# Optimization experiments

Measured on AMD Instinct MI355X. Metric: run time of the kernel, lower is better.

## Reference

```python
import jax, jax.numpy as jnp
import numpy as np

N_NODES = 50000
N_EDGES = 600000
D_IN = 128
D = 128
N_REL = 2
N_LAYERS = 3


def rgcn_conv(h, src, dst, edge_type, weight, root, bias):
    # PyG RGCNConv (no bases), aggr='mean' per relation:
    # out_i = h_i @ root + bias + sum_r mean_{j in N_r(i)} h_j @ W_r
    out = h @ root + bias                      # [N, D]
    hs = h[src]                                # [E, D] gather once
    for r in range(N_REL):
        mask = (edge_type == r).astype(h.dtype)          # [E]
        agg = jax.ops.segment_sum(hs * mask[:, None], dst, num_segments=N_NODES)  # [N, D]
        cnt = jax.ops.segment_sum(mask, dst, num_segments=N_NODES)                # [N]
        mean = agg / jnp.maximum(cnt, 1.0)[:, None]
        out = out + mean @ weight[r]
    return out


def setup_inputs() -> dict:
    key = jax.random.key(0)
    ks = jax.random.split(key, 10)
    x = jax.random.normal(ks[0], (N_NODES, D_IN), dtype=jnp.float32)
    edge_index = jax.random.randint(ks[1], (2, N_EDGES), 0, N_NODES, dtype=jnp.int64)
    edge_attr = jax.random.normal(ks[2], (N_EDGES, N_REL), dtype=jnp.float32)
    # input projection f: Linear(D_IN, D); stored as [D_IN, D] (apply as x @ Wf + bf)
    Wf = jax.random.normal(ks[3], (D_IN, D), dtype=jnp.float32) / np.sqrt(D_IN)
    bf = jnp.zeros((D,), dtype=jnp.float32)
    # per-layer RGCNConv params, stacked over layers
    conv_weight = jax.random.normal(ks[4], (N_LAYERS, N_REL, D, D), dtype=jnp.float32) / np.sqrt(D)
    conv_root = jax.random.normal(ks[5], (N_LAYERS, D, D), dtype=jnp.float32) / np.sqrt(D)
    conv_bias = jnp.zeros((N_LAYERS, D), dtype=jnp.float32)
    return {"x": x, "edge_index": edge_index, "edge_attr": edge_attr,
            "Wf": Wf, "bf": bf, "conv_weight": conv_weight,
            "conv_root": conv_root, "conv_bias": conv_bias}


def reference(x, edge_index, edge_attr, Wf, bf, conv_weight, conv_root, conv_bias):
    src, dst = edge_index[0], edge_index[1]
    edge_type = jnp.argmax(edge_attr, axis=1)           # [E]
    h = jax.nn.relu(x @ Wf + bf)                        # [N, D]
    for l in range(N_LAYERS):
        h = rgcn_conv(h, src, dst, edge_type, conv_weight[l], conv_root[l], conv_bias[l])
        h = jax.nn.relu(h)
    return h
```

## Files before the change

### kernel.cpp

```cpp
#include <hip/hip_runtime.h>
#include <hip/hip_bf16.h>

#define NN 50000
#define NE 600000
#define D 128
#define NREL 2
#define BM 128

typedef __attribute__((ext_vector_type(8))) short bf16x8;
typedef __attribute__((ext_vector_type(4))) float f32x4;

__device__ __forceinline__ float bf2f(short s) {
    return __uint_as_float(((unsigned int)(unsigned short)s) << 16);
}

__global__ void k_etype_count(const float* __restrict__ attr,
                              const int* __restrict__ dst,
                              int* __restrict__ etype,
                              int* __restrict__ cnt, int E) {
    int i = blockIdx.x * blockDim.x + threadIdx.x;
    if (i >= E) return;
    float2 a = reinterpret_cast<const float2*>(attr)[i];
    int r = (a.y > a.x) ? 1 : 0;
    etype[i] = r;
    atomicAdd(&cnt[r * NN + dst[i]], 1);
}

__global__ void k_inv(const int* __restrict__ cnt, float* __restrict__ inv) {
    int i = blockIdx.x * blockDim.x + threadIdx.x;
    if (i >= NREL * NN) return;
    int c = cnt[i];
    inv[i] = 1.0f / (float)(c > 1 ? c : 1);
}

__global__ void k_alloc(const int* __restrict__ cnt, int* __restrict__ off,
                        int* __restrict__ total) {
    int i = blockIdx.x * blockDim.x + threadIdx.x;
    if (i >= NREL * NN) return;
    off[i] = atomicAdd(total, cnt[i]);
}

__global__ void k_fill(const int* __restrict__ src, const int* __restrict__ dst,
                       const int* __restrict__ etype,
                       int* __restrict__ cursor, int* __restrict__ srcs, int E) {
    int i = blockIdx.x * blockDim.x + threadIdx.x;
    if (i >= E) return;
    int key = etype[i] * NN + dst[i];
    int pos = atomicAdd(&cursor[key], 1);
    srcs[pos] = src[i];
}

__global__ void k_cvt_x(const float* __restrict__ x,
                        __hip_bfloat16* __restrict__ xb, int n4) {
    int i = blockIdx.x * blockDim.x + threadIdx.x;
    if (i >= n4) return;
    float4 v = reinterpret_cast<const float4*>(x)[i];
    __hip_bfloat162 a = __float22bfloat162_rn(make_float2(v.x, v.y));
    __hip_bfloat162 b = __float22bfloat162_rn(make_float2(v.z, v.w));
    reinterpret_cast<__hip_bfloat162*>(xb)[i * 2 + 0] = a;
    reinterpret_cast<__hip_bfloat162*>(xb)[i * 2 + 1] = b;
}

__global__ void k_prep_w(const float* __restrict__ Wf,
                         const float* __restrict__ cw,
                         const float* __restrict__ cr,
                         __hip_bfloat16* __restrict__ wt) {
    int idx = blockIdx.x * blockDim.x + threadIdx.x;
    if (idx >= 16384 + 3 * 49152) return;
    float v;
    if (idx < 16384) {
        int n = idx >> 7, k = idx & 127;
        v = Wf[k * 128 + n];
    } else {
        int j = idx - 16384;
        int l = j / 49152; j %= 49152;
        int n = j / 384, k = j % 384;
        if (k < 128)      v = cr[((size_t)l * 128 + k) * 128 + n];
        else if (k < 256) v = cw[((size_t)(l * 2 + 0) * 128 + (k - 128)) * 128 + n];
        else              v = cw[((size_t)(l * 2 + 1) * 128 + (k - 256)) * 128 + n];
    }
    wt[idx] = __float2bfloat16(v);
}

__global__ __launch_bounds__(256)
void k_aggregate(const __hip_bfloat16* __restrict__ h,
                 const int* __restrict__ srcs,
                 const int* __restrict__ off, const int* __restrict__ cnt,
                 const float* __restrict__ inv,
                 __hip_bfloat16* __restrict__ agg) {
    int wid = (blockIdx.x * blockDim.x + threadIdx.x) >> 6;
    int lane = threadIdx.x & 63;
    if (wid >= NREL * NN) return;
    int start = off[wid], c = cnt[wid];
    int g = lane >> 4, l16 = lane & 15;

    int sv = (lane < c) ? srcs[start + lane] : 0;

    float acc[8];
#pragma unroll
    for (int i = 0; i < 8; i++) acc[i] = 0.f;

    for (int base = 0; base < c; base += 8) {
        int j0 = base + g, j1 = base + g + 4;
        int t0 = __shfl(sv, j0 & 63);
        int t1 = __shfl(sv, j1 & 63);
        int s0 = (j0 < 64) ? t0 : ((j0 < c) ? srcs[start + j0] : 0);
        int s1 = (j1 < 64) ? t1 : ((j1 < c) ? srcs[start + j1] : 0);
        if (j0 < c) {
            bf16x8 v0 = *reinterpret_cast<const bf16x8*>(
                h + (size_t)s0 * D + l16 * 8);
#pragma unroll
            for (int i = 0; i < 8; i++) acc[i] += bf2f(v0[i]);
        }
        if (j1 < c) {
            bf16x8 v1 = *reinterpret_cast<const bf16x8*>(
                h + (size_t)s1 * D + l16 * 8);
#pragma unroll
            for (int i = 0; i < 8; i++) acc[i] += bf2f(v1[i]);
        }
    }

#pragma unroll
    for (int i = 0; i < 8; i++) acc[i] += __shfl_xor(acc[i], 16);
#pragma unroll
    for (int i = 0; i < 8; i++) acc[i] += __shfl_xor(acc[i], 32);

    if (g == 0) {
        float sc = inv[wid];
        union { bf16x8 v; __hip_bfloat162 h2[4]; } o;
#pragma unroll
        for (int i = 0; i < 4; i++)
            o.h2[i] = __float22bfloat162_rn(
                make_float2(acc[2 * i] * sc, acc[2 * i + 1] * sc));
        *reinterpret_cast<bf16x8*>(agg + (size_t)wid * D + l16 * 8) = o.v;
    }
}

template <int KTOT, bool OUT_F32>
__global__ __launch_bounds__(256)
void k_gemm_mfma(const __hip_bfloat16* __restrict__ A0,
                 const __hip_bfloat16* __restrict__ A1,
                 const __hip_bfloat16* __restrict__ A2,
                 const __hip_bfloat16* __restrict__ Wt,
                 const float* __restrict__ bias,
                 void* __restrict__ outv, int N) {
    __shared__ uint4 sB4[1024];
    char* sB = (char*)sB4;
    const int tid = threadIdx.x;
    const int w = tid >> 6;
    const int l16 = tid & 15, lg = (tid & 63) >> 4;
    const __hip_bfloat16* As[3] = {A0, A1, A2};

    f32x4 acc[2][8];
#pragma unroll
    for (int m = 0; m < 2; m++)
#pragma unroll
        for (int n = 0; n < 8; n++) acc[m][n] = (f32x4)(0.f);

    const size_t row0 = (size_t)blockIdx.x * BM;
    const int NKB = KTOT / 64;
#pragma unroll
    for (int kb = 0; kb < NKB; ++kb) {
        const __hip_bfloat16* Ac = As[kb >> 1];
        const int koff = (kb & 1) * 64;
        bf16x8 afr[2][2];
#pragma unroll
        for (int mb = 0; mb < 2; ++mb)
#pragma unroll
            for (int kk = 0; kk < 2; ++kk) {
                int r = (int)row0 + w * 32 + mb * 16 + l16;
                if (r >= N) r = N - 1;
                afr[mb][kk] = *reinterpret_cast<const bf16x8*>(
                    Ac + (size_t)r * D + koff + kk * 32 + lg * 8);
            }
        __syncthreads();
        {
            int trow = tid >> 3;
            int tb = (tid & 7) * 16;
#pragma unroll
            for (int p = 0; p < 4; ++p) {
                int rr = trow + p * 32;
                uint4 v = *reinterpret_cast<const uint4*>(
                    (const char*)(Wt + (size_t)rr * KTOT + kb * 64) + tb);
                *reinterpret_cast<uint4*>(sB + rr * 128 + (tb ^ ((rr & 7) << 4))) = v;
            }
        }
        __syncthreads();
#pragma unroll
        for (int kk = 0; kk < 2; ++kk) {
#pragma unroll
            for (int nb = 0; nb < 8; ++nb) {
                int brow = nb * 16 + l16;
                int bcol = kk * 64 + lg * 16;
                bf16x8 bfr = *reinterpret_cast<const bf16x8*>(
                    sB + brow * 128 + (bcol ^ ((brow & 7) << 4)));
                acc[0][nb] = __builtin_amdgcn_mfma_f32_16x16x32_bf16(
                    afr[0][kk], bfr, acc[0][nb], 0, 0, 0);
                acc[1][nb] = __builtin_amdgcn_mfma_f32_16x16x32_bf16(
                    afr[1][kk], bfr, acc[1][nb], 0, 0, 0);
            }
        }
    }
#pragma unroll
    for (int nb = 0; nb < 8; ++nb) {
        int n = nb * 16 + l16;
        float bv = bias[n];
#pragma unroll
        for (int mb = 0; mb < 2; ++mb) {
#pragma unroll
            for (int r = 0; r < 4; ++r) {
                long grow = (long)row0 + w * 32 + mb * 16 + lg * 4 + r;
                if (grow < N) {
                    float v = acc[mb][nb][r] + bv;
                    v = v > 0.f ? v : 0.f;
                    if (OUT_F32)
                        ((float*)outv)[(size_t)grow * D + n] = v;
                    else
                        ((__hip_bfloat16*)outv)[(size_t)grow * D + n] =
                            __float2bfloat16(v);
                }
            }
        }
    }
}

extern "C" void kernel_launch(void* const* d_in, const int* in_sizes, int n_in,
                              void* d_out, int out_size, void* d_ws, size_t ws_size,
                              hipStream_t stream) {
    const float* x    = (const float*)d_in[0];
    const int*   ei   = (const int*)d_in[1];
    const float* attr = (const float*)d_in[2];
    const float* Wf   = (const float*)d_in[3];
    const float* bf   = (const float*)d_in[4];
    const float* cw   = (const float*)d_in[5];
    const float* cr   = (const float*)d_in[6];
    const float* cb   = (const float*)d_in[7];
    const int* src  = ei;
    const int* dstv = ei + NE;

    char* p = (char*)d_ws;
    __hip_bfloat16* h0   = (__hip_bfloat16*)p; p += (size_t)NN * D * 2;
    __hip_bfloat16* h1   = (__hip_bfloat16*)p; p += (size_t)NN * D * 2;
    __hip_bfloat16* aggb = (__hip_bfloat16*)p; p += (size_t)2 * NN * D * 2;
    __hip_bfloat16* xb   = (__hip_bfloat16*)p; p += (size_t)NN * D * 2;
    __hip_bfloat16* wt   = (__hip_bfloat16*)p; p += (size_t)(16384 + 3 * 49152) * 2;
    float* inv  = (float*)p;                p += (size_t)2 * NN * 4;
    int*   cnt  = (int*)p;                  p += (size_t)2 * NN * 4;
    int*   etyp = (int*)p;                  p += (size_t)NE * 4;
    int*   off  = (int*)p;                  p += (size_t)2 * NN * 4;
    int*   cur  = (int*)p;                  p += (size_t)2 * NN * 4;
    int*   srcs = (int*)p;                  p += (size_t)NE * 4;
    int*   total= (int*)p;

    float* outp = (float*)d_out;

    hipMemsetAsync(cnt, 0, (size_t)2 * NN * sizeof(int), stream);
    hipMemsetAsync(total, 0, sizeof(int), stream);
    k_etype_count<<<(NE + 255) / 256, 256, 0, stream>>>(attr, dstv, etyp, cnt, NE);
    k_inv<<<(2 * NN + 255) / 256, 256, 0, stream>>>(cnt, inv);
    k_alloc<<<(2 * NN + 255) / 256, 256, 0, stream>>>(cnt, off, total);
    hipMemcpyAsync(cur, off, (size_t)2 * NN * sizeof(int),
                   hipMemcpyDeviceToDevice, stream);
    k_fill<<<(NE + 255) / 256, 256, 0, stream>>>(src, dstv, etyp, cur, srcs, NE);
    k_cvt_x<<<(NN * D / 4 + 255) / 256, 256, 0, stream>>>(x, xb, NN * D / 4);
    k_prep_w<<<(16384 + 3 * 49152 + 255) / 256, 256, 0, stream>>>(Wf, cw, cr, wt);

    const int gblocks = (NN + BM - 1) / BM;
    k_gemm_mfma<128, false><<<gblocks, 256, 0, stream>>>(
        xb, xb, xb, wt, bf, h0, NN);

    const int ablocks = (2 * NN * 64 + 255) / 256;
    for (int l = 0; l < 3; ++l) {
        const __hip_bfloat16* hin = (l == 1) ? h1 : h0;
        k_aggregate<<<ablocks, 256, 0, stream>>>(hin, srcs, off, cnt, inv, aggb);
        const __hip_bfloat16* wl = wt + 16384 + (size_t)l * 49152;
        const float* bl = cb + (size_t)l * D;
        if (l == 2) {
            k_gemm_mfma<384, true><<<gblocks, 256, 0, stream>>>(
                hin, aggb, aggb + (size_t)NN * D, wl, bl, outp, NN);
        } else {
            __hip_bfloat16* hout = (l == 0) ? h1 : h0;
            k_gemm_mfma<384, false><<<gblocks, 256, 0, stream>>>(
                hin, aggb, aggb + (size_t)NN * D, wl, bl, hout, NN);
        }
    }
}
```

Baseline: 284.0 us.

## Fuse preprocessing kernels, fold x conversion into projection GEMM, unroll aggregation gathers

Merges edge-type counting with weight prep into one launch, and merges the inverse-count, offset-allocation and cursor copy into a second launch. The edge-type buffer is dropped by recomputing the argmax inside the fill kernel. A dedicated projection GEMM reads fp32 x directly and converts it to bf16 in registers, which removes the separate conversion pass and its bf16 copy of x. The aggregation loop now issues four independent row loads per iteration instead of two to raise memory-level parallelism, at the cost of reading row 0 for masked-out slots.

```diff
diff --git a/kernel.cpp b/kernel.cpp
--- a/kernel.cpp
+++ b/kernel.cpp
@@ -13,73 +13,71 @@
 __device__ __forceinline__ float bf2f(short s) {
     return __uint_as_float(((unsigned int)(unsigned short)s) << 16);
 }
-
-__global__ void k_etype_count(const float* __restrict__ attr,
-                              const int* __restrict__ dst,
-                              int* __restrict__ etype,
-                              int* __restrict__ cnt, int E) {
+__device__ __forceinline__ bf16x8 pack_bf8(const float* a) {
+    union { bf16x8 v; __hip_bfloat162 h2[4]; } o;
+#pragma unroll
+    for (int i = 0; i < 4; i++)
+        o.h2[i] = __float22bfloat162_rn(make_float2(a[2 * i], a[2 * i + 1]));
+    return o.v;
+}
+
+#define NEB ((NE + 255) / 256)
+#define NWT (16384 + 3 * 49152)
+#define NWB ((NWT + 255) / 256)
+
+__global__ void k_pre1(const float* __restrict__ attr,
+                       const int* __restrict__ dst,
+                       int* __restrict__ cnt,
+                       const float* __restrict__ Wf,
+                       const float* __restrict__ cw,
+                       const float* __restrict__ cr,
+                       __hip_bfloat16* __restrict__ wt) {
+    if (blockIdx.x < NEB) {
+        int i = blockIdx.x * blockDim.x + threadIdx.x;
+        if (i >= NE) return;
+        float2 a = reinterpret_cast<const float2*>(attr)[i];
+        int r = (a.y > a.x) ? 1 : 0;
+        atomicAdd(&cnt[r * NN + dst[i]], 1);
+    } else {
+        int idx = (blockIdx.x - NEB) * blockDim.x + threadIdx.x;
+        if (idx >= NWT) return;
+        float v;
+        if (idx < 16384) {
+            int n = idx >> 7, k = idx & 127;
+            v = Wf[k * 128 + n];
+        } else {
+            int j = idx - 16384;
+            int l = j / 49152; j %= 49152;
+            int n = j / 384, k = j % 384;
+            if (k < 128)      v = cr[((size_t)l * 128 + k) * 128 + n];
+            else if (k < 256) v = cw[((size_t)(l * 2 + 0) * 128 + (k - 128)) * 128 + n];
+            else              v = cw[((size_t)(l * 2 + 1) * 128 + (k - 256)) * 128 + n];
+        }
+        wt[idx] = __float2bfloat16(v);
+    }
+}
+
+__global__ void k_pre2(const int* __restrict__ cnt, float* __restrict__ inv,
+                       int* __restrict__ off, int* __restrict__ cur,
+                       int* __restrict__ total) {
+    int i = blockIdx.x * blockDim.x + threadIdx.x;
+    if (i >= NREL * NN) return;
+    int c = cnt[i];
+    inv[i] = 1.0f / (float)(c > 1 ? c : 1);
+    int o = atomicAdd(total, c);
+    off[i] = o;
+    cur[i] = o;
+}
+
+__global__ void k_fill(const float* __restrict__ attr,
+                       const int* __restrict__ src, const int* __restrict__ dst,
+                       int* __restrict__ cursor, int* __restrict__ srcs, int E) {
     int i = blockIdx.x * blockDim.x + threadIdx.x;
     if (i >= E) return;
     float2 a = reinterpret_cast<const float2*>(attr)[i];
     int r = (a.y > a.x) ? 1 : 0;
-    etype[i] = r;
-    atomicAdd(&cnt[r * NN + dst[i]], 1);
-}
-
-__global__ void k_inv(const int* __restrict__ cnt, float* __restrict__ inv) {
-    int i = blockIdx.x * blockDim.x + threadIdx.x;
-    if (i >= NREL * NN) return;
-    int c = cnt[i];
-    inv[i] = 1.0f / (float)(c > 1 ? c : 1);
-}
-
-__global__ void k_alloc(const int* __restrict__ cnt, int* __restrict__ off,
-                        int* __restrict__ total) {
-    int i = blockIdx.x * blockDim.x + threadIdx.x;
-    if (i >= NREL * NN) return;
-    off[i] = atomicAdd(total, cnt[i]);
-}
-
-__global__ void k_fill(const int* __restrict__ src, const int* __restrict__ dst,
-                       const int* __restrict__ etype,
-                       int* __restrict__ cursor, int* __restrict__ srcs, int E) {
-    int i = blockIdx.x * blockDim.x + threadIdx.x;
-    if (i >= E) return;
-    int key = etype[i] * NN + dst[i];
-    int pos = atomicAdd(&cursor[key], 1);
+    int pos = atomicAdd(&cursor[r * NN + dst[i]], 1);
     srcs[pos] = src[i];
-}
-
-__global__ void k_cvt_x(const float* __restrict__ x,
-                        __hip_bfloat16* __restrict__ xb, int n4) {
-    int i = blockIdx.x * blockDim.x + threadIdx.x;
-    if (i >= n4) return;
-    float4 v = reinterpret_cast<const float4*>(x)[i];
-    __hip_bfloat162 a = __float22bfloat162_rn(make_float2(v.x, v.y));
-    __hip_bfloat162 b = __float22bfloat162_rn(make_float2(v.z, v.w));
-    reinterpret_cast<__hip_bfloat162*>(xb)[i * 2 + 0] = a;
-    reinterpret_cast<__hip_bfloat162*>(xb)[i * 2 + 1] = b;
-}
-
-__global__ void k_prep_w(const float* __restrict__ Wf,
-                         const float* __restrict__ cw,
-                         const float* __restrict__ cr,
-                         __hip_bfloat16* __restrict__ wt) {
-    int idx = blockIdx.x * blockDim.x + threadIdx.x;
-    if (idx >= 16384 + 3 * 49152) return;
-    float v;
-    if (idx < 16384) {
-        int n = idx >> 7, k = idx & 127;
-        v = Wf[k * 128 + n];
-    } else {
-        int j = idx - 16384;
-        int l = j / 49152; j %= 49152;
-        int n = j / 384, k = j % 384;
-        if (k < 128)      v = cr[((size_t)l * 128 + k) * 128 + n];
-        else if (k < 256) v = cw[((size_t)(l * 2 + 0) * 128 + (k - 128)) * 128 + n];
-        else              v = cw[((size_t)(l * 2 + 1) * 128 + (k - 256)) * 128 + n];
-    }
-    wt[idx] = __float2bfloat16(v);
 }
 
 __global__ __launch_bounds__(256)
@@ -100,23 +98,24 @@
 #pragma unroll
     for (int i = 0; i < 8; i++) acc[i] = 0.f;
 
-    for (int base = 0; base < c; base += 8) {
-        int j0 = base + g, j1 = base + g + 4;
-        int t0 = __shfl(sv, j0 & 63);
-        int t1 = __shfl(sv, j1 & 63);
-        int s0 = (j0 < 64) ? t0 : ((j0 < c) ? srcs[start + j0] : 0);
-        int s1 = (j1 < 64) ? t1 : ((j1 < c) ? srcs[start + j1] : 0);
-        if (j0 < c) {
-            bf16x8 v0 = *reinterpret_cast<const bf16x8*>(
-                h + (size_t)s0 * D + l16 * 8);
-#pragma unroll
-            for (int i = 0; i < 8; i++) acc[i] += bf2f(v0[i]);
-        }
-        if (j1 < c) {
-            bf16x8 v1 = *reinterpret_cast<const bf16x8*>(
-                h + (size_t)s1 * D + l16 * 8);
-#pragma unroll
-            for (int i = 0; i < 8; i++) acc[i] += bf2f(v1[i]);
+    for (int base = 0; base < c; base += 16) {
+        int s[4];
+#pragma unroll
+        for (int q = 0; q < 4; q++) {
+            int jj = base + g + q * 4;
+            int t = __shfl(sv, jj & 63);
+            s[q] = (jj < 64) ? t : ((jj < c) ? srcs[start + jj] : 0);
+            if (jj >= c) s[q] = 0;
+        }
+        bf16x8 v[4];
+#pragma unroll
+        for (int q = 0; q < 4; q++)
+            v[q] = *reinterpret_cast<const bf16x8*>(h + (size_t)s[q] * D + l16 * 8);
+#pragma unroll
+        for (int q = 0; q < 4; q++) {
+            bool ok = (base + g + q * 4) < c;
+#pragma unroll
+            for (int i = 0; i < 8; i++) acc[i] += ok ? bf2f(v[q][i]) : 0.f;
         }
     }
 
@@ -127,12 +126,87 @@
 
     if (g == 0) {
         float sc = inv[wid];
-        union { bf16x8 v; __hip_bfloat162 h2[4]; } o;
-#pragma unroll
-        for (int i = 0; i < 4; i++)
-            o.h2[i] = __float22bfloat162_rn(
-                make_float2(acc[2 * i] * sc, acc[2 * i + 1] * sc));
-        *reinterpret_cast<bf16x8*>(agg + (size_t)wid * D + l16 * 8) = o.v;
+        float t[8];
+#pragma unroll
+        for (int i = 0; i < 8; i++) t[i] = acc[i] * sc;
+        *reinterpret_cast<bf16x8*>(agg + (size_t)wid * D + l16 * 8) = pack_bf8(t);
+    }
+}
+
+__global__ __launch_bounds__(256)
+void k_gemm_proj(const float* __restrict__ X,
+                 const __hip_bfloat16* __restrict__ Wt,
+                 const float* __restrict__ bias,
+                 __hip_bfloat16* __restrict__ out, int N) {
+    __shared__ uint4 sB4[1024];
+    char* sB = (char*)sB4;
+    const int tid = threadIdx.x;
+    const int w = tid >> 6;
+    const int l16 = tid & 15, lg = (tid & 63) >> 4;
+
+    f32x4 acc[2][8];
+#pragma unroll
+    for (int m = 0; m < 2; m++)
+#pragma unroll
+        for (int n = 0; n < 8; n++) acc[m][n] = (f32x4)(0.f);
+
+    const int row0 = blockIdx.x * 128;
+#pragma unroll
+    for (int kb = 0; kb < 2; ++kb) {
+        bf16x8 afr[2][2];
+#pragma unroll
+        for (int mb = 0; mb < 2; ++mb)
+#pragma unroll
+            for (int kk = 0; kk < 2; ++kk) {
+                int r = row0 + w * 32 + mb * 16 + l16;
+                if (r >= N) r = N - 1;
+                const float* p = X + (size_t)r * D + kb * 64 + kk * 32 + lg * 8;
+                float4 u0 = reinterpret_cast<const float4*>(p)[0];
+                float4 u1 = reinterpret_cast<const float4*>(p)[1];
+                float t[8] = {u0.x, u0.y, u0.z, u0.w, u1.x, u1.y, u1.z, u1.w};
+                afr[mb][kk] = pack_bf8(t);
+            }
+        __syncthreads();
+        {
+            int trow = tid >> 3, tb = (tid & 7) * 16;
+#pragma unroll
+            for (int p = 0; p < 4; ++p) {
+                int rr = trow + p * 32;
+                uint4 v = *reinterpret_cast<const uint4*>(
+                    (const char*)(Wt + (size_t)rr * 128 + kb * 64) + tb);
+                *reinterpret_cast<uint4*>(sB + rr * 128 + (tb ^ ((rr & 7) << 4))) = v;
+            }
+        }
+        __syncthreads();
+#pragma unroll
+        for (int kk = 0; kk < 2; ++kk)
+#pragma unroll
+            for (int nb = 0; nb < 8; ++nb) {
+                int brow = nb * 16 + l16;
+                int bcol = kk * 64 + lg * 16;
+                bf16x8 bfr = *reinterpret_cast<const bf16x8*>(
+                    sB + brow * 128 + (bcol ^ ((brow & 7) << 4)));
+                acc[0][nb] = __builtin_amdgcn_mfma_f32_16x16x32_bf16(
+                    afr[0][kk], bfr, acc[0][nb], 0, 0, 0);
+                acc[1][nb] = __builtin_amdgcn_mfma_f32_16x16x32_bf16(
+                    afr[1][kk], bfr, acc[1][nb], 0, 0, 0);
+            }
+    }
+#pragma unroll
+    for (int nb = 0; nb < 8; ++nb) {
+        int n = nb * 16 + l16;
+        float bv = bias[n];
+#pragma unroll
+        for (int mb = 0; mb < 2; ++mb)
+#pragma unroll
+            for (int r = 0; r < 4; ++r) {
+                int grow = row0 + w * 32 + mb * 16 + lg * 4 + r;
+                if (grow < N) {
+                    float v = acc[mb][nb][r] + bv;
+                    v = v > 0.f ? v : 0.f;
+                    out[(size_t)grow * D + n] = __float2bfloat16(v);
+                }
+            }
     }
 }
 
@@ -242,11 +316,9 @@
     __hip_bfloat16* h0   = (__hip_bfloat16*)p; p += (size_t)NN * D * 2;
     __hip_bfloat16* h1   = (__hip_bfloat16*)p; p += (size_t)NN * D * 2;
     __hip_bfloat16* aggb = (__hip_bfloat16*)p; p += (size_t)2 * NN * D * 2;
-    __hip_bfloat16* xb   = (__hip_bfloat16*)p; p += (size_t)NN * D * 2;
-    __hip_bfloat16* wt   = (__hip_bfloat16*)p; p += (size_t)(16384 + 3 * 49152) * 2;
+    __hip_bfloat16* wt   = (__hip_bfloat16*)p; p += (size_t)NWT * 2;
     float* inv  = (float*)p;                p += (size_t)2 * NN * 4;
     int*   cnt  = (int*)p;                  p += (size_t)2 * NN * 4;
-    int*   etyp = (int*)p;                  p += (size_t)NE * 4;
     int*   off  = (int*)p;                  p += (size_t)2 * NN * 4;
     int*   cur  = (int*)p;                  p += (size_t)2 * NN * 4;
     int*   srcs = (int*)p;                  p += (size_t)NE * 4;
@@ -256,19 +328,13 @@
 
     hipMemsetAsync(cnt, 0, (size_t)2 * NN * sizeof(int), stream);
     hipMemsetAsync(total, 0, sizeof(int), stream);
-    k_etype_count<<<(NE + 255) / 256, 256, 0, stream>>>(attr, dstv, etyp, cnt, NE);
-    k_inv<<<(2 * NN + 255) / 256, 256, 0, stream>>>(cnt, inv);
-    k_alloc<<<(2 * NN + 255) / 256, 256, 0, stream>>>(cnt, off, total);
-    hipMemcpyAsync(cur, off, (size_t)2 * NN * sizeof(int),
-                   hipMemcpyDeviceToDevice, stream);
-    k_fill<<<(NE + 255) / 256, 256, 0, stream>>>(src, dstv, etyp, cur, srcs, NE);
-    k_cvt_x<<<(NN * D / 4 + 255) / 256, 256, 0, stream>>>(x, xb, NN * D / 4);
-    k_prep_w<<<(16384 + 3 * 49152 + 255) / 256, 256, 0, stream>>>(Wf, cw, cr, wt);
+    k_pre1<<<NEB + NWB, 256, 0, stream>>>(attr, dstv, cnt, Wf, cw, cr, wt);
+    k_pre2<<<(2 * NN + 255) / 256, 256, 0, stream>>>(cnt, inv, off, cur, total);
+    k_fill<<<NEB, 256, 0, stream>>>(attr, src, dstv, cur, srcs, NE);
+
+    k_gemm_proj<<<(NN + 127) / 128, 256, 0, stream>>>(x, wt, bf, h0, NN);
 
     const int gblocks = (NN + BM - 1) / BM;
-    k_gemm_mfma<128, false><<<gblocks, 256, 0, stream>>>(
-        xb, xb, xb, wt, bf, h0, NN);
-
     const int ablocks = (2 * NN * 64 + 255) / 256;
     for (int l = 0; l < 3; ++l) {
         const __hip_bfloat16* hin = (l == 1) ? h1 : h0;
```

New measurement: 271.1 us. 1.05x faster.
